# Kernel tuning notes

Measured on AMD Instinct MI355X. Metric: run time of the kernel, lower is better.

Reference implementation:

```python
import jax, jax.numpy as jnp
import numpy as np

MARGIN = 0.5


def setup_inputs() -> dict:
    key = jax.random.key(0)
    k1, k2, k3, k4 = jax.random.split(key, 4)
    Ns, Nt, D = 8192, 8192, 512
    return {
        "source_emb": jax.random.normal(k1, (Ns, D), dtype=jnp.float32),
        "target_emb": jax.random.normal(k2, (Nt, D), dtype=jnp.float32),
        "source_sec": jax.random.randint(k3, (Ns,), 0, 6),
        "target_sec": jax.random.randint(k4, (Nt,), 0, 6),
    }


def reference(source_emb, target_emb, source_sec, target_sec):
    D = source_emb.shape[-1]
    Nt = target_emb.shape[0]
    sq_s = jnp.sum(source_emb * source_emb, axis=-1)  # [Ns]
    sq_t = jnp.sum(target_emb * target_emb, axis=-1)  # [Nt]
    gram = jnp.einsum("sd,td->st", source_emb, target_emb)  # [Ns, Nt]
    d2 = jnp.maximum(sq_s[:, None] + sq_t[None, :] - 2.0 * gram, 0.0) / D
    d = jnp.sqrt(d2)
    same = source_sec[:, None] == target_sec[None, :]  # [Ns, Nt] bool
    # semantic: sum of d^2 over matching pairs, divided by Nt
    loss_s = jnp.sum(jnp.where(same, d2, 0.0), axis=1) / Nt
    # contrastive: sum of max(0, margin - d)^2 over non-matching pairs, / Nt
    hinge = jnp.maximum(0.0, MARGIN - d) ** 2
    loss_c = jnp.sum(jnp.where(same, 0.0, hinge), axis=1) / Nt
    return (loss_s, loss_c)
```

## Files before the change

kernel.cpp:

```cpp
#include <hip/hip_runtime.h>
#include <stdint.h>
#include <stddef.h>

#define NS 8192
#define NT 8192
#define DD 512
#define NSEC 6
#define QS 32.0f
#define INV_S2 (1.0f / (QS * QS))
#define INV_DNT (1.0f / ((float)DD * (float)NT))
#define INV_NT  (1.0f / (float)NT)

typedef __attribute__((ext_vector_type(4))) int i32x4;
typedef __attribute__((ext_vector_type(16))) int i32x16;

#define WS_A    ((size_t)0)
#define WS_B    (WS_A + (size_t)NS * DD)
#define WS_SQS  (WS_B + (size_t)NT * DD)
#define WS_SQT  (WS_SQS + (size_t)NS * 4)
#define WS_TS   (WS_SQT + (size_t)NT * 4)
#define WS_CNT  (WS_TS + (size_t)NSEC * DD * 4)
#define WS_SSQ  (WS_CNT + NSEC * 4)
#define WS_ZEND (WS_SSQ + NSEC * 4)

__device__ __forceinline__ void gload16(const void* g, void* l) {
  __builtin_amdgcn_global_load_lds(
      (const __attribute__((address_space(1))) unsigned int*)g,
      (__attribute__((address_space(3))) unsigned int*)l, 16, 0, 0);
}

__global__ __launch_bounds__(256) void prep_kernel(
    const float* __restrict__ src, const float* __restrict__ tgt,
    char* __restrict__ ws) {
  const int tid = threadIdx.x, wid = tid >> 6, lane = tid & 63;
  char* Ai8 = ws + WS_A;
  char* Bi8 = ws + WS_B;
  float* sqs = (float*)(ws + WS_SQS);
  float* sqt = (float*)(ws + WS_SQT);

  if (blockIdx.x == 0) {
    int* Z = (int*)(ws + WS_TS);
    for (int i = tid; i < (int)((WS_ZEND - WS_TS) >> 2); i += 256) Z[i] = 0;
  }

#pragma unroll
  for (int it = 0; it < 4; ++it) {
    const int row = blockIdx.x * 4 + wid + it * 4096;
    const bool isT = row >= NS;
    const int r = isT ? row - NS : row;
    const float* in = (isT ? tgt : src) + (size_t)r * DD;
    const float4* rp = (const float4*)in;
    float4 v0 = rp[lane * 2], v1 = rp[lane * 2 + 1];
    float x[8] = {v0.x, v0.y, v0.z, v0.w, v1.x, v1.y, v1.z, v1.w};
    float ss = 0.f;
    int q[8];
#pragma unroll
    for (int j = 0; j < 8; ++j) {
      ss += x[j] * x[j];
      int qi = __float2int_rn(x[j] * QS);
      q[j] = min(127, max(-127, qi));
    }
    const int lo = (q[0] & 255) | ((q[1] & 255) << 8) |
                   ((q[2] & 255) << 16) | ((q[3] & 255) << 24);
    const int hi = (q[4] & 255) | ((q[5] & 255) << 8) |
                   ((q[6] & 255) << 16) | ((q[7] & 255) << 24);
    *(int2*)((isT ? Bi8 : Ai8) + (size_t)r * DD + lane * 8) = make_int2(lo, hi);
#pragma unroll
    for (int off = 32; off >= 1; off >>= 1) ss += __shfl_xor(ss, off, 64);
    if (lane == 0) (isT ? sqt : sqs)[r] = ss;
  }
}

__global__ __launch_bounds__(512) void tsumq_kernel(
    const int* __restrict__ tsec, char* __restrict__ ws) {
  const int d = threadIdx.x;
  const int r0 = blockIdx.x * 64;
  const signed char* B = (const signed char*)(ws + WS_B);
  int a[NSEC] = {0, 0, 0, 0, 0, 0};
#pragma unroll 4
  for (int r = 0; r < 64; ++r) {
    const int sec = tsec[r0 + r];
    const int v = (int)B[(size_t)(r0 + r) * DD + d];
#pragma unroll
    for (int c = 0; c < NSEC; ++c) a[c] += (sec == c) ? v : 0;
  }
  int* T = (int*)(ws + WS_TS);
#pragma unroll
  for (int c = 0; c < NSEC; ++c) atomicAdd(&T[c * DD + d], a[c]);

  if (threadIdx.x < 64) {
    const float* sqt = (const float*)(ws + WS_SQT);
    const int r = r0 + threadIdx.x;
    const int sec = tsec[r];
    const float qv = sqt[r];
    float cn[NSEC], sq[NSEC];
#pragma unroll
    for (int c = 0; c < NSEC; ++c) {
      cn[c] = (sec == c) ? 1.f : 0.f;
      sq[c] = (sec == c) ? qv : 0.f;
    }
#pragma unroll
    for (int c = 0; c < NSEC; ++c) {
#pragma unroll
      for (int off = 32; off >= 1; off >>= 1) {
        cn[c] += __shfl_xor(cn[c], off, 64);
        sq[c] += __shfl_xor(sq[c], off, 64);
      }
    }
    if (threadIdx.x == 0) {
      float* cnt = (float*)(ws + WS_CNT);
      float* ssq = (float*)(ws + WS_SSQ);
#pragma unroll
      for (int c = 0; c < NSEC; ++c) {
        atomicAdd(&cnt[c], cn[c]);
        atomicAdd(&ssq[c], sq[c]);
      }
    }
  }
}

__global__ __launch_bounds__(256) void ls_kernel(
    const int* __restrict__ ssec, const char* __restrict__ ws,
    float* __restrict__ out) {
  const int tid = threadIdx.x, wid = tid >> 6, lane = tid & 63;
  const int row = blockIdx.x * 4 + wid;
  const int c = ssec[row];
  const signed char* A = (const signed char*)(ws + WS_A);
  const int* T = (const int*)(ws + WS_TS) + c * DD;

  union { int2 v; signed char b[8]; } u;
  u.v = *(const int2*)(A + (size_t)row * DD + lane * 8);
  i32x4 t0 = *(const i32x4*)(T + lane * 8);
  i32x4 t1 = *(const i32x4*)(T + lane * 8 + 4);
  int s = (int)u.b[0] * t0[0] + (int)u.b[1] * t0[1] +
          (int)u.b[2] * t0[2] + (int)u.b[3] * t0[3] +
          (int)u.b[4] * t1[0] + (int)u.b[5] * t1[1] +
          (int)u.b[6] * t1[2] + (int)u.b[7] * t1[3];
#pragma unroll
  for (int off = 32; off >= 1; off >>= 1) s += __shfl_xor(s, off, 64);

  if (lane == 0) {
    const float* cnt = (const float*)(ws + WS_CNT);
    const float* ssq = (const float*)(ws + WS_SSQ);
    const float* sqs = (const float*)(ws + WS_SQS);
    out[row] = (cnt[c] * sqs[row] + ssq[c] - (float)s * (1.0f / 512.0f)) *
               INV_DNT;
    out[NS + row] = 0.f;
  }
}

__global__ __launch_bounds__(256, 2) void gram_kernel(
    const char* __restrict__ ws, const int* __restrict__ ssec,
    const int* __restrict__ tsec, float* __restrict__ out) {
  __shared__ __align__(16) char lds[3][24576];

  const float* sqs = (const float*)(ws + WS_SQS);
  const float* sqt = (const float*)(ws + WS_SQT);

  const int lin = blockIdx.x;
  const int xcd = lin & 7, ii = lin >> 3;
  const int m_blk = xcd * 8 + (ii & 7);
  const int n_blk = ii >> 3;
  const int rowA = m_blk * 128, rowB = n_blk * 256;

  const int tid = threadIdx.x, wid = tid >> 6, lane = tid & 63;
  const int wr = wid >> 1, wc = wid & 1;
  const int lh = lane >> 5;

  const char* aSrc[2];
  const char* bSrc[4];
  int aDst[2], bDst[4];
#pragma unroll
  for (int ih = 0; ih < 2; ++ih) {
    const int o = ih * 4096 + tid * 16;
    const int row_p = o >> 6;
    const int bl = (o & 63) ^ (((row_p >> 1) & 3) << 4);
    aDst[ih] = ih * 4096 + wid * 1024;
    aSrc[ih] = ws + WS_A + (size_t)(rowA + row_p) * DD + bl;
  }
#pragma unroll
  for (int ih = 0; ih < 4; ++ih) {
    const int o = ih * 4096 + tid * 16;
    const int row_p = o >> 6;
    const int bl = (o & 63) ^ (((row_p >> 1) & 3) << 4);
    bDst[ih] = 8192 + ih * 4096 + wid * 1024;
    bSrc[ih] = ws + WS_B + (size_t)(rowB + row_p) * DD + bl;
  }

#define STAGE(T, BUF)                                             \
  {                                                               \
    gload16(aSrc[0] + (size_t)(T) * 64, &lds[BUF][aDst[0]]);      \
    gload16(aSrc[1] + (size_t)(T) * 64, &lds[BUF][aDst[1]]);      \
    gload16(bSrc[0] + (size_t)(T) * 64, &lds[BUF][bDst[0]]);      \
    gload16(bSrc[1] + (size_t)(T) * 64, &lds[BUF][bDst[1]]);      \
    gload16(bSrc[2] + (size_t)(T) * 64, &lds[BUF][bDst[2]]);      \
    gload16(bSrc[3] + (size_t)(T) * 64, &lds[BUF][bDst[3]]);      \
  }

  int aOff[2][2], bOff[4][2];
#pragma unroll
  for (int kk = 0; kk < 2; ++kk) {
    const int l = kk * 32 + lh * 16;
#pragma unroll
    for (int mi = 0; mi < 2; ++mi) {
      const int ra = wr * 64 + mi * 32 + (lane & 31);
      aOff[mi][kk] = ra * 64 + (l ^ (((ra >> 1) & 3) << 4));
    }
#pragma unroll
    for (int ni = 0; ni < 4; ++ni) {
      const int rb = wc * 128 + ni * 32 + (lane & 31);
      bOff[ni][kk] = 8192 + rb * 64 + (l ^ (((rb >> 1) & 3) << 4));
    }
  }

  i32x16 acc[2][4];
#pragma unroll
  for (int mi = 0; mi < 2; ++mi)
#pragma unroll
    for (int ni = 0; ni < 4; ++ni)
#pragma unroll
      for (int j = 0; j < 16; ++j) acc[mi][ni][j] = 0;

  STAGE(0, 0)
  STAGE(1, 1)
  asm volatile("s_waitcnt vmcnt(6)" ::: "memory");
  __builtin_amdgcn_sched_barrier(0);
  __builtin_amdgcn_s_barrier();

#pragma unroll
  for (int t = 0; t < 8; ++t) {
    const int cur = t % 3;
    if (t + 2 < 8) STAGE(t + 2, (t + 2) % 3)

    i32x4 a[2][2], b[4][2];
#pragma unroll
    for (int kk = 0; kk < 2; ++kk) {
#pragma unroll
      for (int mi = 0; mi < 2; ++mi)
        a[mi][kk] = *(const i32x4*)&lds[cur][aOff[mi][kk]];
#pragma unroll
      for (int ni = 0; ni < 4; ++ni)
        b[ni][kk] = *(const i32x4*)&lds[cur][bOff[ni][kk]];
    }
#pragma unroll
    for (int kk = 0; kk < 2; ++kk)
#pragma unroll
      for (int mi = 0; mi < 2; ++mi)
#pragma unroll
        for (int ni = 0; ni < 4; ++ni)
          acc[mi][ni] = __builtin_amdgcn_mfma_i32_32x32x32_i8(
              a[mi][kk], b[ni][kk], acc[mi][ni], 0, 0, 0);

    __builtin_amdgcn_sched_barrier(0);
    if (t + 2 < 8) {
      asm volatile("s_waitcnt vmcnt(6)" ::: "memory");
    } else if (t == 6) {
      asm volatile("s_waitcnt vmcnt(0)" ::: "memory");
    }
    __builtin_amdgcn_sched_barrier(0);
    if (t < 7) __builtin_amdgcn_s_barrier();
  }
#undef STAGE

  const int colc = lane & 31;
  float sqc[4];
#pragma unroll
  for (int ni = 0; ni < 4; ++ni)
    sqc[ni] = sqt[rowB + wc * 128 + ni * 32 + colc];

  float smin = sqs[rowA + wr * 64 + lane];
#pragma unroll
  for (int off = 32; off >= 1; off >>= 1)
    smin = fminf(smin, __shfl_xor(smin, off, 64));

  int thr[4];
#pragma unroll
  for (int ni = 0; ni < 4; ++ni)
    thr[ni] = (int)((smin + sqc[ni] - 129.0f) * 512.0f);

  int mx[4] = {(int)0x80000000, (int)0x80000000,
               (int)0x80000000, (int)0x80000000};
#pragma unroll
  for (int mi = 0; mi < 2; ++mi)
#pragma unroll
    for (int ni = 0; ni < 4; ++ni)
#pragma unroll
      for (int j = 0; j < 16; ++j) mx[ni] = max(mx[ni], acc[mi][ni][j]);

  const bool fire = (mx[0] > thr[0]) || (mx[1] > thr[1]) ||
                    (mx[2] > thr[2]) || (mx[3] > thr[3]);
  if (__any(fire)) {
#pragma unroll
    for (int mi = 0; mi < 2; ++mi) {
#pragma unroll
      for (int j = 0; j < 16; ++j) {
        const int rowin = (j & 3) + 8 * (j >> 2) + 4 * lh;
        const int grow = rowA + wr * 64 + mi * 32 + rowin;
        const float sqr = sqs[grow];
        const int sc = ssec[grow];
#pragma unroll
        for (int ni = 0; ni < 4; ++ni) {
          const int gcol = rowB + wc * 128 + ni * 32 + colc;
          const float d2r =
              sqr + sqc[ni] - 2.f * (float)acc[mi][ni][j] * INV_S2;
          if (d2r < 128.f) {
            if (sc != tsec[gcol]) {
              const float d = sqrtf(fmaxf(d2r, 0.f) * (1.f / (float)DD));
              const float hh = 0.5f - d;
              atomicAdd(&out[NS + grow], hh * hh * INV_NT);
            } else if (d2r < 0.f) {
              atomicAdd(&out[grow], -d2r * INV_DNT);
            }
          }
        }
      }
    }
  }
}

extern "C" void kernel_launch(void* const* d_in, const int* in_sizes, int n_in,
                              void* d_out, int out_size, void* d_ws, size_t ws_size,
                              hipStream_t stream) {
  const float* src = (const float*)d_in[0];
  const float* tgt = (const float*)d_in[1];
  const int* ssec = (const int*)d_in[2];
  const int* tsec = (const int*)d_in[3];
  float* out = (float*)d_out;
  char* ws = (char*)d_ws;

  prep_kernel<<<1024, 256, 0, stream>>>(src, tgt, ws);
  tsumq_kernel<<<128, 512, 0, stream>>>(tsec, ws);
  ls_kernel<<<2048, 256, 0, stream>>>(ssec, ws, out);
  gram_kernel<<<2048, 256, 0, stream>>>(ws, ssec, tsec, out);
}
```

Measured before the change: 79.81 us.

## Shrink gram tile, stream A operands into registers, raise occupancy

The gram kernel tile is cut from 128x256 to 128x128 and the grid doubled. Only B is staged in LDS through a triple buffer; A fragments are loaded straight from global memory into double-buffered registers. With LDS down to 24KB, launch bounds now ask for 3 blocks per CU, and MFMA issue is wrapped in raised wave priority. The tsumq kernel is split into twice as many 32-row blocks for more parallelism. The trade-off is more global re-reads of B across tiles and reliance on implicit vmcnt ordering for LDS readiness.

New measurement: 129.9 us. 62.8% more time.

```diff
diff --git a/kernel.cpp b/kernel.cpp
--- a/kernel.cpp
+++ b/kernel.cpp
@@ -74,11 +74,11 @@
 __global__ __launch_bounds__(512) void tsumq_kernel(
     const int* __restrict__ tsec, char* __restrict__ ws) {
   const int d = threadIdx.x;
-  const int r0 = blockIdx.x * 64;
+  const int r0 = blockIdx.x * 32;
   const signed char* B = (const signed char*)(ws + WS_B);
   int a[NSEC] = {0, 0, 0, 0, 0, 0};
 #pragma unroll 4
-  for (int r = 0; r < 64; ++r) {
+  for (int r = 0; r < 32; ++r) {
     const int sec = tsec[r0 + r];
     const int v = (int)B[(size_t)(r0 + r) * DD + d];
 #pragma unroll
@@ -88,7 +88,7 @@
 #pragma unroll
   for (int c = 0; c < NSEC; ++c) atomicAdd(&T[c * DD + d], a[c]);
 
-  if (threadIdx.x < 64) {
+  if (threadIdx.x < 32) {
     const float* sqt = (const float*)(ws + WS_SQT);
     const int r = r0 + threadIdx.x;
     const int sec = tsec[r];
@@ -102,7 +102,7 @@
 #pragma unroll
     for (int c = 0; c < NSEC; ++c) {
 #pragma unroll
-      for (int off = 32; off >= 1; off >>= 1) {
+      for (int off = 16; off >= 1; off >>= 1) {
         cn[c] += __shfl_xor(cn[c], off, 64);
         sq[c] += __shfl_xor(sq[c], off, 64);
       }
@@ -149,10 +149,10 @@
   }
 }
 
-__global__ __launch_bounds__(256, 2) void gram_kernel(
+__global__ __launch_bounds__(256, 3) void gram_kernel(
     const char* __restrict__ ws, const int* __restrict__ ssec,
     const int* __restrict__ tsec, float* __restrict__ out) {
-  __shared__ __align__(16) char lds[3][24576];
+  __shared__ __align__(16) char ldsB[3][8192];
 
   const float* sqs = (const float*)(ws + WS_SQS);
   const float* sqt = (const float*)(ws + WS_SQT);
@@ -161,135 +161,132 @@
   const int xcd = lin & 7, ii = lin >> 3;
   const int m_blk = xcd * 8 + (ii & 7);
   const int n_blk = ii >> 3;
-  const int rowA = m_blk * 128, rowB = n_blk * 256;
+  const int rowA = m_blk * 128, rowB = n_blk * 128;
 
   const int tid = threadIdx.x, wid = tid >> 6, lane = tid & 63;
   const int wr = wid >> 1, wc = wid & 1;
-  const int lh = lane >> 5;
-
-  const char* aSrc[2];
-  const char* bSrc[4];
-  int aDst[2], bDst[4];
+  const int lh = lane >> 5, l31 = lane & 31;
+
+  const char* bSrc[2];
+  int bDst[2];
 #pragma unroll
   for (int ih = 0; ih < 2; ++ih) {
     const int o = ih * 4096 + tid * 16;
     const int row_p = o >> 6;
     const int bl = (o & 63) ^ (((row_p >> 1) & 3) << 4);
-    aDst[ih] = ih * 4096 + wid * 1024;
-    aSrc[ih] = ws + WS_A + (size_t)(rowA + row_p) * DD + bl;
-  }
-#pragma unroll
-  for (int ih = 0; ih < 4; ++ih) {
-    const int o = ih * 4096 + tid * 16;
-    const int row_p = o >> 6;
-    const int bl = (o & 63) ^ (((row_p >> 1) & 3) << 4);
-    bDst[ih] = 8192 + ih * 4096 + wid * 1024;
+    bDst[ih] = ih * 4096 + wid * 1024;
     bSrc[ih] = ws + WS_B + (size_t)(rowB + row_p) * DD + bl;
   }
 
-#define STAGE(T, BUF)                                             \
+  int bOff[2][2];
+#pragma unroll
+  for (int ni = 0; ni < 2; ++ni)
+#pragma unroll
+    for (int kk = 0; kk < 2; ++kk) {
+      const int rb = wc * 64 + ni * 32 + l31;
+      bOff[ni][kk] = rb * 64 + ((kk * 32 + lh * 16) ^ (((rb >> 1) & 3) << 4));
+    }
+
+  const char* aPtr[2][2];
+#pragma unroll
+  for (int mi = 0; mi < 2; ++mi)
+#pragma unroll
+    for (int kk = 0; kk < 2; ++kk)
+      aPtr[mi][kk] = ws + WS_A +
+                     (size_t)(rowA + wr * 64 + mi * 32 + l31) * DD +
+                     kk * 32 + lh * 16;
+
+  i32x16 acc[2][2];
+#pragma unroll
+  for (int mi = 0; mi < 2; ++mi)
+#pragma unroll
+    for (int ni = 0; ni < 2; ++ni)
+#pragma unroll
+      for (int j = 0; j < 16; ++j) acc[mi][ni][j] = 0;
+
+  i32x4 areg[2][2][2];
+
+#define STAGEB(T, BUF)                                            \
   {                                                               \
-    gload16(aSrc[0] + (size_t)(T) * 64, &lds[BUF][aDst[0]]);      \
-    gload16(aSrc[1] + (size_t)(T) * 64, &lds[BUF][aDst[1]]);      \
-    gload16(bSrc[0] + (size_t)(T) * 64, &lds[BUF][bDst[0]]);      \
-    gload16(bSrc[1] + (size_t)(T) * 64, &lds[BUF][bDst[1]]);      \
-    gload16(bSrc[2] + (size_t)(T) * 64, &lds[BUF][bDst[2]]);      \
-    gload16(bSrc[3] + (size_t)(T) * 64, &lds[BUF][bDst[3]]);      \
-  }
-
-  int aOff[2][2], bOff[4][2];
-#pragma unroll
-  for (int kk = 0; kk < 2; ++kk) {
-    const int l = kk * 32 + lh * 16;
-#pragma unroll
-    for (int mi = 0; mi < 2; ++mi) {
-      const int ra = wr * 64 + mi * 32 + (lane & 31);
-      aOff[mi][kk] = ra * 64 + (l ^ (((ra >> 1) & 3) << 4));
-    }
-#pragma unroll
-    for (int ni = 0; ni < 4; ++ni) {
-      const int rb = wc * 128 + ni * 32 + (lane & 31);
-      bOff[ni][kk] = 8192 + rb * 64 + (l ^ (((rb >> 1) & 3) << 4));
-    }
-  }
-
-  i32x16 acc[2][4];
-#pragma unroll
-  for (int mi = 0; mi < 2; ++mi)
-#pragma unroll
-    for (int ni = 0; ni < 4; ++ni)
-#pragma unroll
-      for (int j = 0; j < 16; ++j) acc[mi][ni][j] = 0;
-
-  STAGE(0, 0)
-  STAGE(1, 1)
+    gload16(bSrc[0] + (size_t)(T) * 64, &ldsB[BUF][bDst[0]]);     \
+    gload16(bSrc[1] + (size_t)(T) * 64, &ldsB[BUF][bDst[1]]);     \
+  }
+#define LOADA(T, BUF)                                             \
+  {                                                               \
+    _Pragma("unroll") for (int mi = 0; mi < 2; ++mi)              \
+      _Pragma("unroll") for (int kk = 0; kk < 2; ++kk)            \
+        areg[BUF][mi][kk] =                                       \
+            *(const i32x4*)(aPtr[mi][kk] + (size_t)(T) * 64);     \
+  }
+
+  STAGEB(0, 0)
+  STAGEB(1, 1)
+  __builtin_amdgcn_sched_barrier(0);
+  LOADA(0, 0)
   asm volatile("s_waitcnt vmcnt(6)" ::: "memory");
   __builtin_amdgcn_sched_barrier(0);
   __builtin_amdgcn_s_barrier();
+  __builtin_amdgcn_sched_barrier(0);
 
 #pragma unroll
   for (int t = 0; t < 8; ++t) {
-    const int cur = t % 3;
-    if (t + 2 < 8) STAGE(t + 2, (t + 2) % 3)
-
-    i32x4 a[2][2], b[4][2];
-#pragma unroll
-    for (int kk = 0; kk < 2; ++kk) {
+    if (t + 2 < 8) STAGEB(t + 2, (t + 2) % 3)
+    __builtin_amdgcn_sched_barrier(0);
+
+    i32x4 b[2][2];
+#pragma unroll
+    for (int ni = 0; ni < 2; ++ni)
+#pragma unroll
+      for (int kk = 0; kk < 2; ++kk)
+        b[ni][kk] = *(const i32x4*)&ldsB[t % 3][bOff[ni][kk]];
+
+    if (t + 1 < 8) LOADA(t + 1, (t + 1) & 1)
+
+    __builtin_amdgcn_s_setprio(1);
+#pragma unroll
+    for (int kk = 0; kk < 2; ++kk)
 #pragma unroll
       for (int mi = 0; mi < 2; ++mi)
-        a[mi][kk] = *(const i32x4*)&lds[cur][aOff[mi][kk]];
-#pragma unroll
-      for (int ni = 0; ni < 4; ++ni)
-        b[ni][kk] = *(const i32x4*)&lds[cur][bOff[ni][kk]];
-    }
-#pragma unroll
-    for (int kk = 0; kk < 2; ++kk)
-#pragma unroll
-      for (int mi = 0; mi < 2; ++mi)
-#pragma unroll
-        for (int ni = 0; ni < 4; ++ni)
+#pragma unroll
+        for (int ni = 0; ni < 2; ++ni)
           acc[mi][ni] = __builtin_amdgcn_mfma_i32_32x32x32_i8(
-              a[mi][kk], b[ni][kk], acc[mi][ni], 0, 0, 0);
-
-    __builtin_amdgcn_sched_barrier(0);
-    if (t + 2 < 8) {
-      asm volatile("s_waitcnt vmcnt(6)" ::: "memory");
-    } else if (t == 6) {
-      asm volatile("s_waitcnt vmcnt(0)" ::: "memory");
-    }
-    __builtin_amdgcn_sched_barrier(0);
-    if (t < 7) __builtin_amdgcn_s_barrier();
-  }
-#undef STAGE
-
-  const int colc = lane & 31;
-  float sqc[4];
-#pragma unroll
-  for (int ni = 0; ni < 4; ++ni)
-    sqc[ni] = sqt[rowB + wc * 128 + ni * 32 + colc];
+              areg[t & 1][mi][kk], b[ni][kk], acc[mi][ni], 0, 0, 0);
+    __builtin_amdgcn_s_setprio(0);
+
+    if (t < 7) {
+      __builtin_amdgcn_sched_barrier(0);
+      __builtin_amdgcn_s_barrier();
+      __builtin_amdgcn_sched_barrier(0);
+    }
+  }
+#undef STAGEB
+#undef LOADA
+
+  float sqc[2];
+#pragma unroll
+  for (int ni = 0; ni < 2; ++ni)
+    sqc[ni] = sqt[rowB + wc * 64 + ni * 32 + l31];
 
   float smin = sqs[rowA + wr * 64 + lane];
 #pragma unroll
   for (int off = 32; off >= 1; off >>= 1)
     smin = fminf(smin, __shfl_xor(smin, off, 64));
 
-  int thr[4];
-#pragma unroll
-  for (int ni = 0; ni < 4; ++ni)
+  int thr[2];
+#pragma unroll
+  for (int ni = 0; ni < 2; ++ni)
     thr[ni] = (int)((smin + sqc[ni] - 129.0f) * 512.0f);
 
-  int mx[4] = {(int)0x80000000, (int)0x80000000,
-               (int)0x80000000, (int)0x80000000};
+  int mx0 = (int)0x80000000, mx1 = (int)0x80000000;
 #pragma unroll
   for (int mi = 0; mi < 2; ++mi)
 #pragma unroll
-    for (int ni = 0; ni < 4; ++ni)
-#pragma unroll
-      for (int j = 0; j < 16; ++j) mx[ni] = max(mx[ni], acc[mi][ni][j]);
-
-  const bool fire = (mx[0] > thr[0]) || (mx[1] > thr[1]) ||
-                    (mx[2] > thr[2]) || (mx[3] > thr[3]);
-  if (__any(fire)) {
+    for (int j = 0; j < 16; ++j) {
+      mx0 = max(mx0, acc[mi][0][j]);
+      mx1 = max(mx1, acc[mi][1][j]);
+    }
+
+  if (__any((mx0 > thr[0]) || (mx1 > thr[1]))) {
 #pragma unroll
     for (int mi = 0; mi < 2; ++mi) {
 #pragma unroll
@@ -299,8 +296,8 @@
         const float sqr = sqs[grow];
         const int sc = ssec[grow];
 #pragma unroll
-        for (int ni = 0; ni < 4; ++ni) {
-          const int gcol = rowB + wc * 128 + ni * 32 + colc;
+        for (int ni = 0; ni < 2; ++ni) {
+          const int gcol = rowB + wc * 64 + ni * 32 + l31;
           const float d2r =
               sqr + sqc[ni] - 2.f * (float)acc[mi][ni][j] * INV_S2;
           if (d2r < 128.f) {
@@ -329,7 +326,7 @@
   char* ws = (char*)d_ws;
 
   prep_kernel<<<1024, 256, 0, stream>>>(src, tgt, ws);
-  tsumq_kernel<<<128, 512, 0, stream>>>(tsec, ws);
+  tsumq_kernel<<<256, 512, 0, stream>>>(tsec, ws);
   ls_kernel<<<2048, 256, 0, stream>>>(ssec, ws, out);
-  gram_kernel<<<2048, 256, 0, stream>>>(ws, ssec, tsec, out);
-}
+  gram_kernel<<<4096, 256, 0, stream>>>(ws, ssec, tsec, out);
+}
```

## Stage full-K A tile in LDS once and stream B directly into registers

Applied to the files above, without the earlier changes.

The gram kernel now loads the whole 128x512 int8 A tile into 64 KiB of LDS up front and reads B fragments directly from global memory into double-buffered registers. This removes the per-step triple-buffered LDS pipeline for B and all block barriers inside the K loop. MFMA blocks are wrapped in s_setprio. The tsumq kernel is also split into twice as many blocks of 32 rows for more parallelism. The tradeoffs are higher register pressure from the B buffers, a larger LDS footprint that may reduce occupancy, and uncoalesced per-lane 16-byte global loads for B.

Result: slower. 126.1 us (+58.0%).

```diff
diff --git a/kernel.cpp b/kernel.cpp
--- a/kernel.cpp
+++ b/kernel.cpp
@@ -74,11 +74,11 @@
 __global__ __launch_bounds__(512) void tsumq_kernel(
     const int* __restrict__ tsec, char* __restrict__ ws) {
   const int d = threadIdx.x;
-  const int r0 = blockIdx.x * 64;
+  const int r0 = blockIdx.x * 32;
   const signed char* B = (const signed char*)(ws + WS_B);
   int a[NSEC] = {0, 0, 0, 0, 0, 0};
 #pragma unroll 4
-  for (int r = 0; r < 64; ++r) {
+  for (int r = 0; r < 32; ++r) {
     const int sec = tsec[r0 + r];
     const int v = (int)B[(size_t)(r0 + r) * DD + d];
 #pragma unroll
@@ -88,7 +88,7 @@
 #pragma unroll
   for (int c = 0; c < NSEC; ++c) atomicAdd(&T[c * DD + d], a[c]);
 
-  if (threadIdx.x < 64) {
+  if (threadIdx.x < 32) {
     const float* sqt = (const float*)(ws + WS_SQT);
     const int r = r0 + threadIdx.x;
     const int sec = tsec[r];
@@ -102,7 +102,7 @@
 #pragma unroll
     for (int c = 0; c < NSEC; ++c) {
 #pragma unroll
-      for (int off = 32; off >= 1; off >>= 1) {
+      for (int off = 16; off >= 1; off >>= 1) {
         cn[c] += __shfl_xor(cn[c], off, 64);
         sq[c] += __shfl_xor(sq[c], off, 64);
       }
@@ -152,7 +152,7 @@
 __global__ __launch_bounds__(256, 2) void gram_kernel(
     const char* __restrict__ ws, const int* __restrict__ ssec,
     const int* __restrict__ tsec, float* __restrict__ out) {
-  __shared__ __align__(16) char lds[3][24576];
+  __shared__ __align__(16) char ldsA[65536];
 
   const float* sqs = (const float*)(ws + WS_SQS);
   const float* sqt = (const float*)(ws + WS_SQT);
@@ -165,53 +165,24 @@
 
   const int tid = threadIdx.x, wid = tid >> 6, lane = tid & 63;
   const int wr = wid >> 1, wc = wid & 1;
-  const int lh = lane >> 5;
-
-  const char* aSrc[2];
-  const char* bSrc[4];
-  int aDst[2], bDst[4];
-#pragma unroll
-  for (int ih = 0; ih < 2; ++ih) {
-    const int o = ih * 4096 + tid * 16;
-    const int row_p = o >> 6;
-    const int bl = (o & 63) ^ (((row_p >> 1) & 3) << 4);
-    aDst[ih] = ih * 4096 + wid * 1024;
-    aSrc[ih] = ws + WS_A + (size_t)(rowA + row_p) * DD + bl;
-  }
-#pragma unroll
-  for (int ih = 0; ih < 4; ++ih) {
-    const int o = ih * 4096 + tid * 16;
-    const int row_p = o >> 6;
-    const int bl = (o & 63) ^ (((row_p >> 1) & 3) << 4);
-    bDst[ih] = 8192 + ih * 4096 + wid * 1024;
-    bSrc[ih] = ws + WS_B + (size_t)(rowB + row_p) * DD + bl;
-  }
-
-#define STAGE(T, BUF)                                             \
-  {                                                               \
-    gload16(aSrc[0] + (size_t)(T) * 64, &lds[BUF][aDst[0]]);      \
-    gload16(aSrc[1] + (size_t)(T) * 64, &lds[BUF][aDst[1]]);      \
-    gload16(bSrc[0] + (size_t)(T) * 64, &lds[BUF][bDst[0]]);      \
-    gload16(bSrc[1] + (size_t)(T) * 64, &lds[BUF][bDst[1]]);      \
-    gload16(bSrc[2] + (size_t)(T) * 64, &lds[BUF][bDst[2]]);      \
-    gload16(bSrc[3] + (size_t)(T) * 64, &lds[BUF][bDst[3]]);      \
-  }
-
-  int aOff[2][2], bOff[4][2];
-#pragma unroll
-  for (int kk = 0; kk < 2; ++kk) {
-    const int l = kk * 32 + lh * 16;
-#pragma unroll
-    for (int mi = 0; mi < 2; ++mi) {
-      const int ra = wr * 64 + mi * 32 + (lane & 31);
-      aOff[mi][kk] = ra * 64 + (l ^ (((ra >> 1) & 3) << 4));
-    }
-#pragma unroll
-    for (int ni = 0; ni < 4; ++ni) {
-      const int rb = wc * 128 + ni * 32 + (lane & 31);
-      bOff[ni][kk] = 8192 + rb * 64 + (l ^ (((rb >> 1) & 3) << 4));
-    }
-  }
+  const int lh = lane >> 5, l31 = lane & 31;
+
+  const int t16 = wid * 1024 + lane * 16;
+  const int r_in = t16 >> 9, o_in = t16 & 511;
+  const char* aStageSrc = ws + WS_A + (size_t)(rowA + r_in) * DD +
+                          (o_in ^ ((r_in & 7) << 4));
+  char* aStageDst = &ldsA[wid * 1024];
+
+  int aBase[2], aMask[2];
+#pragma unroll
+  for (int mi = 0; mi < 2; ++mi) {
+    const int ra = wr * 64 + mi * 32 + l31;
+    aBase[mi] = ra * 512;
+    aMask[mi] = (ra & 7) << 4;
+  }
+
+  const char* bBase = ws + WS_B +
+                      (size_t)(rowB + wc * 128 + l31) * DD + lh * 16;
 
   i32x16 acc[2][4];
 #pragma unroll
@@ -221,27 +192,39 @@
 #pragma unroll
       for (int j = 0; j < 16; ++j) acc[mi][ni][j] = 0;
 
-  STAGE(0, 0)
-  STAGE(1, 1)
-  asm volatile("s_waitcnt vmcnt(6)" ::: "memory");
+  i32x4 breg[2][4][2];
+
+#define LOADB(T, BUF)                                                       \
+  {                                                                         \
+    _Pragma("unroll") for (int ni = 0; ni < 4; ++ni)                        \
+      _Pragma("unroll") for (int kk = 0; kk < 2; ++kk)                      \
+        breg[BUF][ni][kk] = *(const i32x4*)(bBase + ni * 32 * DD +          \
+                                            kk * 32 + (size_t)(T) * 64);    \
+  }
+
+#pragma unroll
+  for (int u = 0; u < 16; ++u)
+    gload16(aStageSrc + u * 4096, aStageDst + u * 4096);
+  __builtin_amdgcn_sched_barrier(0);
+  LOADB(0, 0)
+  asm volatile("s_waitcnt vmcnt(8)" ::: "memory");
   __builtin_amdgcn_sched_barrier(0);
   __builtin_amdgcn_s_barrier();
+  __builtin_amdgcn_sched_barrier(0);
 
 #pragma unroll
   for (int t = 0; t < 8; ++t) {
-    const int cur = t % 3;
-    if (t + 2 < 8) STAGE(t + 2, (t + 2) % 3)
-
-    i32x4 a[2][2], b[4][2];
-#pragma unroll
-    for (int kk = 0; kk < 2; ++kk) {
-#pragma unroll
-      for (int mi = 0; mi < 2; ++mi)
-        a[mi][kk] = *(const i32x4*)&lds[cur][aOff[mi][kk]];
-#pragma unroll
-      for (int ni = 0; ni < 4; ++ni)
-        b[ni][kk] = *(const i32x4*)&lds[cur][bOff[ni][kk]];
-    }
+    if (t + 1 < 8) LOADB(t + 1, (t + 1) & 1)
+
+    i32x4 a[2][2];
+#pragma unroll
+    for (int mi = 0; mi < 2; ++mi)
+#pragma unroll
+      for (int kk = 0; kk < 2; ++kk)
+        a[mi][kk] = *(const i32x4*)&ldsA[aBase[mi] +
+                        ((t * 64 + kk * 32 + lh * 16) ^ aMask[mi])];
+
+    __builtin_amdgcn_s_setprio(1);
 #pragma unroll
     for (int kk = 0; kk < 2; ++kk)
 #pragma unroll
@@ -249,24 +232,16 @@
 #pragma unroll
         for (int ni = 0; ni < 4; ++ni)
           acc[mi][ni] = __builtin_amdgcn_mfma_i32_32x32x32_i8(
-              a[mi][kk], b[ni][kk], acc[mi][ni], 0, 0, 0);
-
+              a[mi][kk], breg[t & 1][ni][kk], acc[mi][ni], 0, 0, 0);
+    __builtin_amdgcn_s_setprio(0);
     __builtin_amdgcn_sched_barrier(0);
-    if (t + 2 < 8) {
-      asm volatile("s_waitcnt vmcnt(6)" ::: "memory");
-    } else if (t == 6) {
-      asm volatile("s_waitcnt vmcnt(0)" ::: "memory");
-    }
-    __builtin_amdgcn_sched_barrier(0);
-    if (t < 7) __builtin_amdgcn_s_barrier();
-  }
-#undef STAGE
-
-  const int colc = lane & 31;
+  }
+#undef LOADB
+
   float sqc[4];
 #pragma unroll
   for (int ni = 0; ni < 4; ++ni)
-    sqc[ni] = sqt[rowB + wc * 128 + ni * 32 + colc];
+    sqc[ni] = sqt[rowB + wc * 128 + ni * 32 + l31];
 
   float smin = sqs[rowA + wr * 64 + lane];
 #pragma unroll
@@ -300,7 +275,7 @@
         const int sc = ssec[grow];
 #pragma unroll
         for (int ni = 0; ni < 4; ++ni) {
-          const int gcol = rowB + wc * 128 + ni * 32 + colc;
+          const int gcol = rowB + wc * 128 + ni * 32 + l31;
           const float d2r =
               sqr + sqc[ni] - 2.f * (float)acc[mi][ni][j] * INV_S2;
           if (d2r < 128.f) {
@@ -329,7 +304,7 @@
   char* ws = (char*)d_ws;
 
   prep_kernel<<<1024, 256, 0, stream>>>(src, tgt, ws);
-  tsumq_kernel<<<128, 512, 0, stream>>>(tsec, ws);
+  tsumq_kernel<<<256, 512, 0, stream>>>(tsec, ws);
   ls_kernel<<<2048, 256, 0, stream>>>(ssec, ws, out);
   gram_kernel<<<2048, 256, 0, stream>>>(ws, ssec, tsec, out);
 }
```
